# Performance work log

Hardware: AMD Instinct MI355X
Metric: run time of the kernel (lower is better)

The kernel has to match this reference:

```python
import jax, jax.numpy as jnp
import numpy as np
from jax import lax


def _lstm_layer(x, W_ih, W_hh, b_ih, b_hh):
    """Single LSTM layer, batch_first x: [B, T, in] -> (out [B,T,H], h_n [B,H], c_n [B,H]).
    PyTorch gate order: i, f, g, o."""
    B, T, _ = x.shape
    H = W_hh.shape[1]
    # Precompute input contributions for all timesteps (one big GEMM).
    xg = jnp.einsum('bti,gi->btg', x, W_ih) + b_ih + b_hh  # [B, T, 4H]
    h0 = jnp.zeros((B, H), dtype=x.dtype)
    c0 = jnp.zeros((B, H), dtype=x.dtype)

    def step(carry, g_t):
        h, c = carry
        gates = g_t + h @ W_hh.T  # [B, 4H]
        i, f, g, o = jnp.split(gates, 4, axis=-1)
        i = jax.nn.sigmoid(i)
        f = jax.nn.sigmoid(f)
        g = jnp.tanh(g)
        o = jax.nn.sigmoid(o)
        c = f * c + i * g
        h = o * jnp.tanh(c)
        return (h, c), h

    (h_n, c_n), hs = lax.scan(step, (h0, c0), jnp.swapaxes(xg, 0, 1))  # hs: [T, B, H]
    return jnp.swapaxes(hs, 0, 1), h_n, c_n


def setup_inputs() -> dict:
    key = jax.random.key(0)
    ks = jax.random.split(key, 12)
    H = 128
    IN = 1
    B, T = 256, 2048
    s = 1.0 / np.sqrt(H)  # PyTorch default init scale

    def u(k, shape):
        return jax.random.uniform(k, shape, jnp.float32, -s, s)

    return {
        'x': jax.random.normal(ks[0], (B, T, IN), jnp.float32),
        'W_ih_l0': u(ks[1], (4 * H, IN)),
        'W_hh_l0': u(ks[2], (4 * H, H)),
        'b_ih_l0': u(ks[3], (4 * H,)),
        'b_hh_l0': u(ks[4], (4 * H,)),
        'W_ih_l1': u(ks[5], (4 * H, H)),
        'W_hh_l1': u(ks[6], (4 * H, H)),
        'b_ih_l1': u(ks[7], (4 * H,)),
        'b_hh_l1': u(ks[8], (4 * H,)),
        'W_fc': u(ks[9], (1, H)),
        'b_fc': u(ks[10], (1,)),
    }


def reference(x, W_ih_l0, W_hh_l0, b_ih_l0, b_hh_l0,
              W_ih_l1, W_hh_l1, b_ih_l1, b_hh_l1, W_fc, b_fc):
    out0, h0, c0 = _lstm_layer(x, W_ih_l0, W_hh_l0, b_ih_l0, b_hh_l0)
    out1, h1, c1 = _lstm_layer(out0, W_ih_l1, W_hh_l1, b_ih_l1, b_hh_l1)
    last = out1[:, -1, :]                 # [B, H]
    y = last @ W_fc.T + b_fc              # [B, 1]
    h_n = jnp.stack([h0, h1], axis=0)     # [num_layers, B, H]
    c_n = jnp.stack([c0, c1], axis=0)
    return (y, h_n, c_n)
```

## Files before the change

### kernel.cpp

```cpp
#include <hip/hip_runtime.h>

#define T_SEQ 2048
#define HDIM  128
#define GDIM  512
#define BATCH 256

typedef _Float16 f16;
typedef _Float16 f16x2 __attribute__((ext_vector_type(2)));
typedef _Float16 f16x8 __attribute__((ext_vector_type(8)));

#if __has_builtin(__builtin_amdgcn_fdot2)
__device__ __forceinline__ float dot2(f16x2 a, f16x2 b, float c) {
    return __builtin_amdgcn_fdot2(a, b, c, false);
}
#else
__device__ __forceinline__ float dot2(f16x2 a, f16x2 b, float c) {
    return c + (float)a[0] * (float)b[0] + (float)a[1] * (float)b[1];
}
#endif

__device__ __forceinline__ f16x2 mk2(float a, float b) {
    f16x2 r; r[0] = (f16)a; r[1] = (f16)b; return r;
}
__device__ __forceinline__ f16x2 pr(f16x8 v, int m) {
    f16x2 r; r[0] = v[2 * m]; r[1] = v[2 * m + 1]; return r;
}

__device__ __forceinline__ float sigm(float x) {
    return __builtin_amdgcn_rcpf(1.0f + __expf(-x));
}
__device__ __forceinline__ float tanh_fast(float x) {
    float e = __expf(2.0f * x);
    return 1.0f - 2.0f * __builtin_amdgcn_rcpf(e + 1.0f);
}

__global__ __launch_bounds__(1024)
void lstm_fused(const float* __restrict__ x,
                const float* __restrict__ Wih0,
                const float* __restrict__ Whh0,
                const float* __restrict__ bih0,
                const float* __restrict__ bhh0,
                const float* __restrict__ Wih1,
                const float* __restrict__ Whh1,
                const float* __restrict__ bih1,
                const float* __restrict__ bhh1,
                const float* __restrict__ Wfc,
                const float* __restrict__ bfc,
                float* __restrict__ out)
{
    __shared__ __align__(16) float xs[T_SEQ];
    __shared__ __align__(16) f16   h0h[HDIM];
    __shared__ __align__(16) f16   h1h[HDIM];
    __shared__ float h0f[HDIM], h1f[HDIM];
    __shared__ float g0[GDIM];
    __shared__ float g1a[GDIM], g1b[GDIM];

    const int t  = threadIdx.x;
    const int b  = blockIdx.x;
    const bool gA = (t < 512);
    const int r  = t & 511;

    if (gA)
        ((float4*)xs)[t] = ((const float4*)(x + (size_t)b * T_SEQ))[t];

    f16x2 wa[64];
    f16x2 wb[32];
    {
        const float4* pa = (const float4*)((gA ? Whh0 : Wih1) + r * HDIM);
        const float4* pb = (const float4*)(Whh1 + r * HDIM + (gA ? 0 : 64));
#pragma unroll
        for (int c = 0; c < 32; ++c) {
            float4 v = pa[c];
            wa[2 * c]     = mk2(v.x, v.y);
            wa[2 * c + 1] = mk2(v.z, v.w);
        }
#pragma unroll
        for (int c = 0; c < 16; ++c) {
            float4 v = pb[c];
            wb[2 * c]     = mk2(v.x, v.y);
            wb[2 * c + 1] = mk2(v.z, v.w);
        }
    }
    const float xw   = gA ? Wih0[r] : 0.f;
    const float bias = gA ? (bih0[r] + bhh0[r]) : (bih1[r] + bhh1[r]);

    if (t < HDIM) {
        h0h[t] = (f16)0.f; h1h[t] = (f16)0.f;
        h0f[t] = 0.f;      h1f[t] = 0.f;
    }
    float c0r = 0.f, c1r = 0.f;
    __syncthreads();

    const f16x8* h0p  = (const f16x8*)h0h;
    const f16x8* hsel = ((const f16x8*)h1h) + (gA ? 0 : 8);

    for (int i = 0; i <= T_SEQ; ++i) {
        float sa = (i < T_SEQ ? xs[i] : 0.f) * xw + bias;
        float sb = 0.f, sc = 0.f, sd = 0.f;
#pragma unroll
        for (int c = 0; c < 16; ++c) {
            f16x8 h = h0p[c];
            sa = dot2(wa[4 * c + 0], pr(h, 0), sa);
            sb = dot2(wa[4 * c + 1], pr(h, 1), sb);
            sa = dot2(wa[4 * c + 2], pr(h, 2), sa);
            sb = dot2(wa[4 * c + 3], pr(h, 3), sb);
        }
#pragma unroll
        for (int c = 0; c < 8; ++c) {
            f16x8 h = hsel[c];
            sc = dot2(wb[4 * c + 0], pr(h, 0), sc);
            sd = dot2(wb[4 * c + 1], pr(h, 1), sd);
            sc = dot2(wb[4 * c + 2], pr(h, 2), sc);
            sd = dot2(wb[4 * c + 3], pr(h, 3), sd);
        }
        if (gA) {
            g0[r]  = sa + sb;
            g1a[r] = sc + sd;
        } else {
            g1b[r] = (sa + sb) + (sc + sd);
        }
        __syncthreads();

        if (t < 128) {
            if (i < T_SEQ) {
                float gi = sigm(g0[t]);
                float gf = sigm(g0[t + 128]);
                float gg = tanh_fast(g0[t + 256]);
                float go = sigm(g0[t + 384]);
                c0r = gf * c0r + gi * gg;
                float h = go * tanh_fast(c0r);
                h0h[t] = (f16)h;
                h0f[t] = h;
            }
        } else if (t >= 512 && t < 640) {
            if (i >= 1) {
                int j = t - 512;
                float gi = sigm(g1a[j]       + g1b[j]);
                float gf = sigm(g1a[j + 128] + g1b[j + 128]);
                float gg = tanh_fast(g1a[j + 256] + g1b[j + 256]);
                float go = sigm(g1a[j + 384] + g1b[j + 384]);
                c1r = gf * c1r + gi * gg;
                float h = go * tanh_fast(c1r);
                h1h[j] = (f16)h;
                h1f[j] = h;
            }
        }
        __syncthreads();
    }

    float* hn = out + BATCH;
    float* cn = out + BATCH + 2 * BATCH * HDIM;
    if (t < 128) {
        hn[(size_t)b * HDIM + t] = h0f[t];
        cn[(size_t)b * HDIM + t] = c0r;
    } else if (t >= 512 && t < 640) {
        int j = t - 512;
        hn[BATCH * HDIM + (size_t)b * HDIM + j] = h1f[j];
        cn[BATCH * HDIM + (size_t)b * HDIM + j] = c1r;
    }
    if (t < 64) {
        float p = h1f[t] * Wfc[t] + h1f[t + 64] * Wfc[t + 64];
#pragma unroll
        for (int o = 32; o >= 1; o >>= 1) p += __shfl_down(p, o);
        if (t == 0) out[b] = p + bfc[0];
    }
}

extern "C" void kernel_launch(void* const* d_in, const int* in_sizes, int n_in,
                              void* d_out, int out_size, void* d_ws, size_t ws_size,
                              hipStream_t stream) {
    const float* x    = (const float*)d_in[0];
    const float* Wih0 = (const float*)d_in[1];
    const float* Whh0 = (const float*)d_in[2];
    const float* bih0 = (const float*)d_in[3];
    const float* bhh0 = (const float*)d_in[4];
    const float* Wih1 = (const float*)d_in[5];
    const float* Whh1 = (const float*)d_in[6];
    const float* bih1 = (const float*)d_in[7];
    const float* bhh1 = (const float*)d_in[8];
    const float* Wfc  = (const float*)d_in[9];
    const float* bfc  = (const float*)d_in[10];
    lstm_fused<<<BATCH, 1024, 0, stream>>>(x, Wih0, Whh0, bih0, bhh0,
                                           Wih1, Whh1, bih1, bhh1,
                                           Wfc, bfc, (float*)d_out);
}
```

Baseline: 3.079 ms.

## Split fused two-layer LSTM into chunked per-layer kernels via workspace

Replaces the single 1024-thread fused kernel with two 512-thread kernels run per time chunk. Layer 0 also computes half of layer 1's input projection and stores it along with the other half of h0 in workspace. Layer 1 then consumes these with a one-step prefetch. Each kernel's recurrence now has a shorter per-step critical path on a smaller block with lower register pressure, so two blocks can share a CU. In exchange, the intermediates make a global-memory round trip and the layers no longer overlap within a block. The fused kernel remains as a fallback when the workspace is too small.

```diff
diff --git a/kernel.cpp b/kernel.cpp
--- a/kernel.cpp
+++ b/kernel.cpp
@@ -25,13 +25,235 @@
 __device__ __forceinline__ f16x2 pr(f16x8 v, int m) {
     f16x2 r; r[0] = v[2 * m]; r[1] = v[2 * m + 1]; return r;
 }
-
 __device__ __forceinline__ float sigm(float x) {
     return __builtin_amdgcn_rcpf(1.0f + __expf(-x));
 }
 __device__ __forceinline__ float tanh_fast(float x) {
     float e = __expf(2.0f * x);
     return 1.0f - 2.0f * __builtin_amdgcn_rcpf(e + 1.0f);
+}
+
+
+__global__ __launch_bounds__(512, 2)
+void lstm_l0(const float* __restrict__ x,
+             const float* __restrict__ Wih0,
+             const float* __restrict__ Whh0,
+             const float* __restrict__ bih0,
+             const float* __restrict__ bhh0,
+             const float* __restrict__ Wih1,
+             const float* __restrict__ bih1,
+             const float* __restrict__ bhh1,
+             float* __restrict__ h0s,  float* __restrict__ c0s,
+             float* __restrict__ xg1p, f16* __restrict__ h0hi,
+             int t0, int len, int first, int last,
+             float* __restrict__ out)
+{
+    __shared__ __align__(16) float xsc[T_SEQ];
+    __shared__ __align__(16) f16   h0h[HDIM];
+    __shared__ float h0f[HDIM];
+    __shared__ float g0[GDIM];
+
+    const int t = threadIdx.x;
+    const int b = blockIdx.x;
+
+    for (int idx = t; idx < len; idx += 512)
+        xsc[idx] = x[(size_t)b * T_SEQ + t0 + idx];
+
+    f16x2 wa[64];
+    f16x2 wb[32];
+    {
+        const float4* pa = (const float4*)(Whh0 + t * HDIM);
+        const float4* pb = (const float4*)(Wih1 + t * HDIM);
+#pragma unroll
+        for (int c = 0; c < 32; ++c) {
+            float4 v = pa[c];
+            wa[2 * c]     = mk2(v.x, v.y);
+            wa[2 * c + 1] = mk2(v.z, v.w);
+        }
+#pragma unroll
+        for (int c = 0; c < 16; ++c) {
+            float4 v = pb[c];
+            wb[2 * c]     = mk2(v.x, v.y);
+            wb[2 * c + 1] = mk2(v.z, v.w);
+        }
+    }
+    const float wx0   = Wih0[t];
+    const float bias0 = bih0[t] + bhh0[t];
+    const float b1    = bih1[t] + bhh1[t];
+
+    float c0r = 0.f;
+    if (t < HDIM) {
+        float h = first ? 0.f : h0s[b * HDIM + t];
+        if (!first) c0r = c0s[b * HDIM + t];
+        h0f[t] = h;
+        h0h[t] = (f16)h;
+    }
+    __syncthreads();
+
+    const f16x8* h0p = (const f16x8*)h0h;
+    float* xgB = xg1p + (size_t)b * len * 512;
+    f16*   hhB = h0hi + (size_t)b * len * 64;
+
+    for (int i = 0; i <= len; ++i) {
+        float s0a = (i < len ? xsc[i] : 0.f) * wx0 + bias0;
+        float s0b = 0.f, s0c = 0.f, s0d = 0.f;
+        float s1a = b1, s1b = 0.f;
+#pragma unroll
+        for (int c = 0; c < 16; ++c) {
+            f16x8 h = h0p[c];
+            s0a = dot2(wa[4 * c + 0], pr(h, 0), s0a);
+            s0b = dot2(wa[4 * c + 1], pr(h, 1), s0b);
+            s0c = dot2(wa[4 * c + 2], pr(h, 2), s0c);
+            s0d = dot2(wa[4 * c + 3], pr(h, 3), s0d);
+            if (c < 8) {
+                s1a = dot2(wb[4 * c + 0], pr(h, 0), s1a);
+                s1b = dot2(wb[4 * c + 1], pr(h, 1), s1b);
+                s1a = dot2(wb[4 * c + 2], pr(h, 2), s1a);
+                s1b = dot2(wb[4 * c + 3], pr(h, 3), s1b);
+            }
+        }
+        if (i < len) g0[t] = (s0a + s0b) + (s0c + s0d);
+        if (i >= 1)  xgB[(size_t)(i - 1) * 512 + t] = s1a + s1b;
+        __syncthreads();
+
+        if (t < 128 && i < len) {
+            float gi = sigm(g0[t]);
+            float gf = sigm(g0[t + 128]);
+            float gg = tanh_fast(g0[t + 256]);
+            float go = sigm(g0[t + 384]);
+            c0r = gf * c0r + gi * gg;
+            float h = go * tanh_fast(c0r);
+            h0h[t] = (f16)h;
+            h0f[t] = h;
+            if (t >= 64) hhB[(size_t)i * 64 + (t - 64)] = (f16)h;
+        }
+        __syncthreads();
+    }
+
+    if (t < 128) {
+        h0s[b * HDIM + t] = h0f[t];
+        c0s[b * HDIM + t] = c0r;
+        if (last) {
+            float* hn = out + BATCH;
+            float* cn = out + BATCH + 2 * BATCH * HDIM;
+            hn[(size_t)b * HDIM + t] = h0f[t];
+            cn[(size_t)b * HDIM + t] = c0r;
+        }
+    }
+}
+
+__global__ __launch_bounds__(512, 2)
+void lstm_l1(const float* __restrict__ Whh1,
+             const float* __restrict__ Wih1,
+             const float* __restrict__ Wfc,
+             const float* __restrict__ bfc,
+             float* __restrict__ h1s, float* __restrict__ c1s,
+             const float* __restrict__ xg1p, const f16* __restrict__ h0hi,
+             int len, int first, int last,
+             float* __restrict__ out)
+{
+    __shared__ __align__(16) f16   h1h[HDIM];
+    __shared__ float h1f[HDIM];
+    __shared__ float g1[GDIM];
+    __shared__ __align__(16) f16   hh[2][64];
+
+    const int t = threadIdx.x;
+    const int b = blockIdx.x;
+
+    f16x2 wa[64];
+    f16x2 wb[32];
+    {
+        const float4* pa = (const float4*)(Whh1 + t * HDIM);
+        const float4* pb = (const float4*)(Wih1 + t * HDIM + 64);
+#pragma unroll
+        for (int c = 0; c < 32; ++c) {
+            float4 v = pa[c];
+            wa[2 * c]     = mk2(v.x, v.y);
+            wa[2 * c + 1] = mk2(v.z, v.w);
+        }
+#pragma unroll
+        for (int c = 0; c < 16; ++c) {
+            float4 v = pb[c];
+            wb[2 * c]     = mk2(v.x, v.y);
+            wb[2 * c + 1] = mk2(v.z, v.w);
+        }
+    }
+
+    float c1r = 0.f;
+    if (t < HDIM) {
+        float h = first ? 0.f : h1s[b * HDIM + t];
+        if (!first) c1r = c1s[b * HDIM + t];
+        h1f[t] = h;
+        h1h[t] = (f16)h;
+    }
+
+    const float* xgB = xg1p + (size_t)b * len * 512;
+    const f16*   hB  = h0hi + (size_t)b * len * 64;
+    if (t < 8) ((f16x8*)hh[0])[t] = ((const f16x8*)hB)[t];
+    float xgv = xgB[t];
+    __syncthreads();
+
+    const f16x8* h1p = (const f16x8*)h1h;
+
+    for (int i = 0; i < len; ++i) {
+        float xgn = 0.f;
+        if (i + 1 < len) {
+            xgn = xgB[(size_t)(i + 1) * 512 + t];
+            if (t < 8)
+                ((f16x8*)hh[(i + 1) & 1])[t] =
+                    ((const f16x8*)(hB + (size_t)(i + 1) * 64))[t];
+        }
+        const f16x8* hhp = (const f16x8*)hh[i & 1];
+
+        float s1a = xgv, s1b = 0.f, s1c = 0.f, s1d = 0.f;
+#pragma unroll
+        for (int c = 0; c < 16; ++c) {
+            f16x8 h = h1p[c];
+            s1a = dot2(wa[4 * c + 0], pr(h, 0), s1a);
+            s1b = dot2(wa[4 * c + 1], pr(h, 1), s1b);
+            s1c = dot2(wa[4 * c + 2], pr(h, 2), s1c);
+            s1d = dot2(wa[4 * c + 3], pr(h, 3), s1d);
+            if (c < 8) {
+                f16x8 hx = hhp[c];
+                s1c = dot2(wb[4 * c + 0], pr(hx, 0), s1c);
+                s1d = dot2(wb[4 * c + 1], pr(hx, 1), s1d);
+                s1c = dot2(wb[4 * c + 2], pr(hx, 2), s1c);
+                s1d = dot2(wb[4 * c + 3], pr(hx, 3), s1d);
+            }
+        }
+        g1[t] = (s1a + s1b) + (s1c + s1d);
+        __syncthreads();
+
+        if (t < 128) {
+            float gi = sigm(g1[t]);
+            float gf = sigm(g1[t + 128]);
+            float gg = tanh_fast(g1[t + 256]);
+            float go = sigm(g1[t + 384]);
+            c1r = gf * c1r + gi * gg;
+            float h = go * tanh_fast(c1r);
+            h1h[t] = (f16)h;
+            h1f[t] = h;
+        }
+        __syncthreads();
+        xgv = xgn;
+    }
+
+    if (t < 128) {
+        h1s[b * HDIM + t] = h1f[t];
+        c1s[b * HDIM + t] = c1r;
+        if (last) {
+            float* hn = out + BATCH;
+            float* cn = out + BATCH + 2 * BATCH * HDIM;
+            hn[BATCH * HDIM + (size_t)b * HDIM + t] = h1f[t];
+            cn[BATCH * HDIM + (size_t)b * HDIM + t] = c1r;
+        }
+    }
+    if (last && t < 64) {
+        float p = h1f[t] * Wfc[t] + h1f[t + 64] * Wfc[t + 64];
+#pragma unroll
+        for (int o = 32; o >= 1; o >>= 1) p += __shfl_down(p, o);
+        if (t == 0) out[b] = p + bfc[0];
+    }
 }
 
 __global__ __launch_bounds__(1024)
@@ -113,12 +335,8 @@
             sc = dot2(wb[4 * c + 2], pr(h, 2), sc);
             sd = dot2(wb[4 * c + 3], pr(h, 3), sd);
         }
-        if (gA) {
-            g0[r]  = sa + sb;
-            g1a[r] = sc + sd;
-        } else {
-            g1b[r] = (sa + sb) + (sc + sd);
-        }
+        if (gA) { g0[r] = sa + sb; g1a[r] = sc + sd; }
+        else    { g1b[r] = (sa + sb) + (sc + sd); }
         __syncthreads();
 
         if (t < 128) {
@@ -180,7 +398,37 @@
     const float* bhh1 = (const float*)d_in[8];
     const float* Wfc  = (const float*)d_in[9];
     const float* bfc  = (const float*)d_in[10];
-    lstm_fused<<<BATCH, 1024, 0, stream>>>(x, Wih0, Whh0, bih0, bhh0,
-                                           Wih1, Whh1, bih1, bhh1,
-                                           Wfc, bfc, (float*)d_out);
-}
+    float* out = (float*)d_out;
+
+    const size_t stateB  = (size_t)4 * BATCH * HDIM * sizeof(float);
+    const size_t perStep = (size_t)BATCH * 512 * 4 + (size_t)BATCH * 64 * 2;
+    long long ch = 0;
+    if (d_ws && ws_size > stateB) ch = (long long)((ws_size - stateB) / perStep);
+    if (ch > T_SEQ) ch = T_SEQ;
+
+    if (ch >= 64) {
+        const int CH = (int)ch;
+        float* h0s  = (float*)d_ws;
+        float* c0s  = h0s + BATCH * HDIM;
+        float* h1s  = c0s + BATCH * HDIM;
+        float* c1s  = h1s + BATCH * HDIM;
+        float* xg1p = c1s + BATCH * HDIM;
+        f16*   h0hi = (f16*)(xg1p + (size_t)BATCH * CH * 512);
+        for (int t0 = 0; t0 < T_SEQ; t0 += CH) {
+            const int len   = (T_SEQ - t0 < CH) ? (T_SEQ - t0) : CH;
+            const int first = (t0 == 0);
+            const int last  = (t0 + len == T_SEQ);
+            lstm_l0<<<BATCH, 512, 0, stream>>>(x, Wih0, Whh0, bih0, bhh0,
+                                               Wih1, bih1, bhh1,
+                                               h0s, c0s, xg1p, h0hi,
+                                               t0, len, first, last, out);
+            lstm_l1<<<BATCH, 512, 0, stream>>>(Whh1, Wih1, Wfc, bfc,
+                                               h1s, c1s, xg1p, h0hi,
+                                               len, first, last, out);
+        }
+    } else {
+        lstm_fused<<<BATCH, 1024, 0, stream>>>(x, Wih0, Whh0, bih0, bhh0,
+                                               Wih1, Whh1, bih1, bhh1,
+                                               Wfc, bfc, out);
+    }
+}
```

After: 3.464 ms. 12.5% more time.

## Use 512-thread blocks with weights split across registers, LDS and global

Applied to the files above, without the earlier changes.

Each block now runs with 512 threads instead of 1024. Every thread computes one gate row for both layers, so a single sum per layer replaces the cross-half partial-sum exchange. The layer-1 weights are spread across three places: registers, a padded LDS tile, and a pre-packed fp16 global buffer built by a small prep kernel and streamed from L2 with software prefetch. The goal is more work per thread and fewer threads per barrier. The cost is higher register pressure, about 140KB of LDS per block, and extra global loads inside the serial time loop.

```diff
diff --git a/kernel.cpp b/kernel.cpp
--- a/kernel.cpp
+++ b/kernel.cpp
@@ -4,6 +4,8 @@
 #define HDIM  128
 #define GDIM  512
 #define BATCH 256
+#define GW_PLANES 8
+#define WS_NEED (GW_PLANES * GDIM * 16)
 
 typedef _Float16 f16;
 typedef _Float16 f16x2 __attribute__((ext_vector_type(2)));
@@ -25,7 +27,12 @@
 __device__ __forceinline__ f16x2 pr(f16x8 v, int m) {
     f16x2 r; r[0] = v[2 * m]; r[1] = v[2 * m + 1]; return r;
 }
-
+__device__ __forceinline__ f16x8 pk8(float4 u, float4 v) {
+    f16x8 w;
+    w[0] = (f16)u.x; w[1] = (f16)u.y; w[2] = (f16)u.z; w[3] = (f16)u.w;
+    w[4] = (f16)v.x; w[5] = (f16)v.y; w[6] = (f16)v.z; w[7] = (f16)v.w;
+    return w;
+}
 __device__ __forceinline__ float sigm(float x) {
     return __builtin_amdgcn_rcpf(1.0f + __expf(-x));
 }
@@ -34,19 +41,210 @@
     return 1.0f - 2.0f * __builtin_amdgcn_rcpf(e + 1.0f);
 }
 
+__global__ void prep_pack(const float* __restrict__ Whh1, f16x8* __restrict__ wg)
+{
+    const int c = blockIdx.x;
+    const int t = threadIdx.x;
+    const float4* s = (const float4*)(Whh1 + t * HDIM + 64 + 8 * c);
+    wg[c * GDIM + t] = pk8(s[0], s[1]);
+}
+
+__global__ __launch_bounds__(512, 2)
+void lstm_fused_v6(const float* __restrict__ x,
+                   const float* __restrict__ Wih0,
+                   const float* __restrict__ Whh0,
+                   const float* __restrict__ bih0,
+                   const float* __restrict__ bhh0,
+                   const float* __restrict__ Wih1,
+                   const float* __restrict__ Whh1,
+                   const float* __restrict__ bih1,
+                   const float* __restrict__ bhh1,
+                   const float* __restrict__ Wfc,
+                   const float* __restrict__ bfc,
+                   const f16x8* __restrict__ wg,
+                   float* __restrict__ out)
+{
+    __shared__ __align__(16) f16x8 wlds[GDIM * 17];
+    __shared__ __align__(16) float xs[T_SEQ];
+    __shared__ __align__(16) f16   h0h[HDIM];
+    __shared__ __align__(16) f16   h1h[HDIM];
+    __shared__ float h0f[HDIM], h1f[HDIM];
+    __shared__ float g0[GDIM], g1[GDIM];
+
+    const int t = threadIdx.x;
+    const int b = blockIdx.x;
+
+    ((float4*)xs)[t] = ((const float4*)(x + (size_t)b * T_SEQ))[t];
+
+    f16x2 w0[64];
+    f16x2 wi[32];
+    {
+        const float4* p0 = (const float4*)(Whh0 + t * HDIM);
+        const float4* p1 = (const float4*)(Wih1 + t * HDIM);
+#pragma unroll
+        for (int c = 0; c < 32; ++c) {
+            float4 v = p0[c];
+            w0[2 * c]     = mk2(v.x, v.y);
+            w0[2 * c + 1] = mk2(v.z, v.w);
+        }
+#pragma unroll
+        for (int c = 0; c < 16; ++c) {
+            float4 v = p1[c];
+            wi[2 * c]     = mk2(v.x, v.y);
+            wi[2 * c + 1] = mk2(v.z, v.w);
+        }
+    }
+    f16x8* wrow = wlds + t * 17;
+    {
+        const float4* p = (const float4*)(Wih1 + t * HDIM + 64);
+#pragma unroll
+        for (int c = 0; c < 8; ++c) wrow[c] = pk8(p[2 * c], p[2 * c + 1]);
+        p = (const float4*)(Whh1 + t * HDIM);
+#pragma unroll
+        for (int c = 0; c < 8; ++c) wrow[8 + c] = pk8(p[2 * c], p[2 * c + 1]);
+    }
+    const float wx0   = Wih0[t];
+    const float bias0 = bih0[t] + bhh0[t];
+    const float bias1 = bih1[t] + bhh1[t];
+
+    if (t < HDIM) {
+        h0h[t] = (f16)0.f; h1h[t] = (f16)0.f;
+        h0f[t] = 0.f;      h1f[t] = 0.f;
+    }
+    float c0r = 0.f, c1r = 0.f;
+    __syncthreads();
+
+    const f16x8* h0p = (const f16x8*)h0h;
+    const f16x8* h1p = (const f16x8*)h1h;
+
+    for (int i = 0; i <= T_SEQ; ++i) {
+        int z = 0;
+        asm volatile("" : "+v"(z));
+        const f16x8* wr  = wrow + z;
+        const f16x8* wg2 = wg + z;
+
+        f16x8 ga = wg2[0 * GDIM + t];
+        f16x8 gb = wg2[1 * GDIM + t];
+
+        float s0a = (i < T_SEQ ? xs[i] : 0.f) * wx0 + bias0;
+        float s0b = 0.f, s0c = 0.f, s0d = 0.f;
+        float s1a = bias1, s1b = 0.f;
+
+#pragma unroll
+        for (int c = 0; c < 8; ++c) {
+            f16x8 h = h0p[c];
+            s0a = dot2(w0[4 * c + 0], pr(h, 0), s0a);
+            s0b = dot2(w0[4 * c + 1], pr(h, 1), s0b);
+            s0c = dot2(w0[4 * c + 2], pr(h, 2), s0c);
+            s0d = dot2(w0[4 * c + 3], pr(h, 3), s0d);
+            s1a = dot2(wi[4 * c + 0], pr(h, 0), s1a);
+            s1b = dot2(wi[4 * c + 1], pr(h, 1), s1b);
+            s1a = dot2(wi[4 * c + 2], pr(h, 2), s1a);
+            s1b = dot2(wi[4 * c + 3], pr(h, 3), s1b);
+        }
+#pragma unroll
+        for (int c = 0; c < 8; ++c) {
+            f16x8 h  = h0p[8 + c];
+            f16x8 lw = wr[c];
+            s0a = dot2(w0[32 + 4 * c + 0], pr(h, 0), s0a);
+            s0b = dot2(w0[32 + 4 * c + 1], pr(h, 1), s0b);
+            s0c = dot2(w0[32 + 4 * c + 2], pr(h, 2), s0c);
+            s0d = dot2(w0[32 + 4 * c + 3], pr(h, 3), s0d);
+            s1a = dot2(pr(lw, 0), pr(h, 0), s1a);
+            s1b = dot2(pr(lw, 1), pr(h, 1), s1b);
+            s1a = dot2(pr(lw, 2), pr(h, 2), s1a);
+            s1b = dot2(pr(lw, 3), pr(h, 3), s1b);
+        }
+#pragma unroll
+        for (int c = 0; c < 8; ++c) {
+            f16x8 h  = h1p[c];
+            f16x8 lw = wr[8 + c];
+            s1a = dot2(pr(lw, 0), pr(h, 0), s1a);
+            s1b = dot2(pr(lw, 1), pr(h, 1), s1b);
+            s1a = dot2(pr(lw, 2), pr(h, 2), s1a);
+            s1b = dot2(pr(lw, 3), pr(h, 3), s1b);
+        }
+#pragma unroll
+        for (int bb = 0; bb < 4; ++bb) {
+            f16x8 na = ga, nb = gb;
+            if (bb < 3) {
+                na = wg2[(2 * bb + 2) * GDIM + t];
+                nb = wg2[(2 * bb + 3) * GDIM + t];
+            }
+            f16x8 h = h1p[8 + 2 * bb];
+            s1a = dot2(pr(ga, 0), pr(h, 0), s1a);
+            s1b = dot2(pr(ga, 1), pr(h, 1), s1b);
+            s1a = dot2(pr(ga, 2), pr(h, 2), s1a);
+            s1b = dot2(pr(ga, 3), pr(h, 3), s1b);
+            h = h1p[9 + 2 * bb];
+            s1a = dot2(pr(gb, 0), pr(h, 0), s1a);
+            s1b = dot2(pr(gb, 1), pr(h, 1), s1b);
+            s1a = dot2(pr(gb, 2), pr(h, 2), s1a);
+            s1b = dot2(pr(gb, 3), pr(h, 3), s1b);
+            ga = na; gb = nb;
+        }
+        g0[t] = (s0a + s0b) + (s0c + s0d);
+        g1[t] = s1a + s1b;
+        __syncthreads();
+
+        if (t < 128) {
+            if (i < T_SEQ) {
+                float gi = sigm(g0[t]);
+                float gf = sigm(g0[t + 128]);
+                float gg = tanh_fast(g0[t + 256]);
+                float go = sigm(g0[t + 384]);
+                c0r = gf * c0r + gi * gg;
+                float h = go * tanh_fast(c0r);
+                h0h[t] = (f16)h;
+                h0f[t] = h;
+            }
+        } else if (t < 256) {
+            if (i >= 1) {
+                int j = t - 128;
+                float gi = sigm(g1[j]);
+                float gf = sigm(g1[j + 128]);
+                float gg = tanh_fast(g1[j + 256]);
+                float go = sigm(g1[j + 384]);
+                c1r = gf * c1r + gi * gg;
+                float h = go * tanh_fast(c1r);
+                h1h[j] = (f16)h;
+                h1f[j] = h;
+            }
+        }
+        __syncthreads();
+    }
+
+    float* hn = out + BATCH;
+    float* cn = out + BATCH + 2 * BATCH * HDIM;
+    if (t < 128) {
+        hn[(size_t)b * HDIM + t] = h0f[t];
+        cn[(size_t)b * HDIM + t] = c0r;
+    } else if (t < 256) {
+        int j = t - 128;
+        hn[BATCH * HDIM + (size_t)b * HDIM + j] = h1f[j];
+        cn[BATCH * HDIM + (size_t)b * HDIM + j] = c1r;
+    }
+    if (t < 64) {
+        float p = h1f[t] * Wfc[t] + h1f[t + 64] * Wfc[t + 64];
+#pragma unroll
+        for (int o = 32; o >= 1; o >>= 1) p += __shfl_down(p, o);
+        if (t == 0) out[b] = p + bfc[0];
+    }
+}
+
 __global__ __launch_bounds__(1024)
-void lstm_fused(const float* __restrict__ x,
-                const float* __restrict__ Wih0,
-                const float* __restrict__ Whh0,
-                const float* __restrict__ bih0,
-                const float* __restrict__ bhh0,
-                const float* __restrict__ Wih1,
-                const float* __restrict__ Whh1,
-                const float* __restrict__ bih1,
-                const float* __restrict__ bhh1,
-                const float* __restrict__ Wfc,
-                const float* __restrict__ bfc,
-                float* __restrict__ out)
+void lstm_fused_fb(const float* __restrict__ x,
+                   const float* __restrict__ Wih0,
+                   const float* __restrict__ Whh0,
+                   const float* __restrict__ bih0,
+                   const float* __restrict__ bhh0,
+                   const float* __restrict__ Wih1,
+                   const float* __restrict__ Whh1,
+                   const float* __restrict__ bih1,
+                   const float* __restrict__ bhh1,
+                   const float* __restrict__ Wfc,
+                   const float* __restrict__ bfc,
+                   float* __restrict__ out)
 {
     __shared__ __align__(16) float xs[T_SEQ];
     __shared__ __align__(16) f16   h0h[HDIM];
@@ -113,12 +311,8 @@
             sc = dot2(wb[4 * c + 2], pr(h, 2), sc);
             sd = dot2(wb[4 * c + 3], pr(h, 3), sd);
         }
-        if (gA) {
-            g0[r]  = sa + sb;
-            g1a[r] = sc + sd;
-        } else {
-            g1b[r] = (sa + sb) + (sc + sd);
-        }
+        if (gA) { g0[r] = sa + sb; g1a[r] = sc + sd; }
+        else    { g1b[r] = (sa + sb) + (sc + sd); }
         __syncthreads();
 
         if (t < 128) {
@@ -180,7 +374,17 @@
     const float* bhh1 = (const float*)d_in[8];
     const float* Wfc  = (const float*)d_in[9];
     const float* bfc  = (const float*)d_in[10];
-    lstm_fused<<<BATCH, 1024, 0, stream>>>(x, Wih0, Whh0, bih0, bhh0,
-                                           Wih1, Whh1, bih1, bhh1,
-                                           Wfc, bfc, (float*)d_out);
-}
+    float* out = (float*)d_out;
+
+    if (d_ws && ws_size >= (size_t)WS_NEED) {
+        f16x8* wg = (f16x8*)d_ws;
+        prep_pack<<<GW_PLANES, GDIM, 0, stream>>>(Whh1, wg);
+        lstm_fused_v6<<<BATCH, GDIM, 0, stream>>>(x, Wih0, Whh0, bih0, bhh0,
+                                                  Wih1, Whh1, bih1, bhh1,
+                                                  Wfc, bfc, wg, out);
+    } else {
+        lstm_fused_fb<<<BATCH, 1024, 0, stream>>>(x, Wih0, Whh0, bih0, bhh0,
+                                                  Wih1, Whh1, bih1, bhh1,
+                                                  Wfc, bfc, out);
+    }
+}
```

Result: faster. 2.964 ms (-3.7%).

## Split LSTM layers into producer/consumer blocks linked by a global-memory FIFO

Applied to the files above, without the earlier changes.

Replaces the single 1024-thread block per batch row with two 512-thread blocks per row: one runs layer 0 and also computes the first half of layer 1's input projection, and the other runs layer 1's recurrence. The two communicate through a 32-deep ring buffer in workspace memory with atomic producer/consumer counters. The aim is to take layer 1 off layer 0's critical path, shorten each block's per-step barrier chain, and run two blocks per CU. The cost is global-memory traffic, spin-waiting, and reliance on both blocks of a pair being co-resident, or the spin-waits deadlock. If the workspace is too small, the old kernel runs as a fallback.

```diff
diff --git a/kernel.cpp b/kernel.cpp
--- a/kernel.cpp
+++ b/kernel.cpp
@@ -5,6 +5,11 @@
 #define GDIM  512
 #define BATCH 256
 
+#define DEPTH    32
+#define SLOT_DW  576
+#define FLAGS_DW 8192
+#define WS_NEED  ((size_t)(FLAGS_DW + (size_t)BATCH * DEPTH * SLOT_DW) * 4)
+
 typedef _Float16 f16;
 typedef _Float16 f16x2 __attribute__((ext_vector_type(2)));
 typedef _Float16 f16x8 __attribute__((ext_vector_type(8)));
@@ -25,7 +30,6 @@
 __device__ __forceinline__ f16x2 pr(f16x8 v, int m) {
     f16x2 r; r[0] = v[2 * m]; r[1] = v[2 * m + 1]; return r;
 }
-
 __device__ __forceinline__ float sigm(float x) {
     return __builtin_amdgcn_rcpf(1.0f + __expf(-x));
 }
@@ -34,19 +38,235 @@
     return 1.0f - 2.0f * __builtin_amdgcn_rcpf(e + 1.0f);
 }
 
+__device__ __forceinline__ uint ldv(const uint* p) {
+    return __hip_atomic_load(p, __ATOMIC_RELAXED, __HIP_MEMORY_SCOPE_AGENT);
+}
+__device__ __forceinline__ void stv(uint* p, uint v) {
+    __hip_atomic_store(p, v, __ATOMIC_RELAXED, __HIP_MEMORY_SCOPE_AGENT);
+}
+
+__global__ __launch_bounds__(512, 2)
+void lstm_pc(const float* __restrict__ x,
+             const float* __restrict__ Wih0,
+             const float* __restrict__ Whh0,
+             const float* __restrict__ bih0,
+             const float* __restrict__ bhh0,
+             const float* __restrict__ Wih1,
+             const float* __restrict__ Whh1,
+             const float* __restrict__ bih1,
+             const float* __restrict__ bhh1,
+             const float* __restrict__ Wfc,
+             const float* __restrict__ bfc,
+             uint* __restrict__ ws,
+             float* __restrict__ out)
+{
+    __shared__ __align__(16) float xs[T_SEQ];
+    __shared__ __align__(16) f16   hsh[HDIM];
+    __shared__ float hsf[HDIM];
+    __shared__ float g[GDIM];
+    __shared__ __align__(16) f16   hh[2][64];
+
+    const int t    = threadIdx.x;
+    const int b    = blockIdx.x >> 1;
+    const int role = blockIdx.x & 1;
+    uint* prod = ws + b * 16;
+    uint* cons = ws + 4096 + b * 16;
+    uint* fif  = ws + FLAGS_DW + (size_t)b * (DEPTH * SLOT_DW);
+
+    float cr = 0.f;
+    if (t < HDIM) { hsh[t] = (f16)0.f; hsf[t] = 0.f; }
+
+    if (role == 0) {
+        ((float4*)xs)[t] = ((const float4*)(x + (size_t)b * T_SEQ))[t];
+        f16x2 wa[64];
+        f16x2 wb[32];
+        {
+            const float4* pa = (const float4*)(Whh0 + t * HDIM);
+            const float4* pb = (const float4*)(Wih1 + t * HDIM);
+#pragma unroll
+            for (int c = 0; c < 32; ++c) {
+                float4 v = pa[c];
+                wa[2*c]   = mk2(v.x, v.y);
+                wa[2*c+1] = mk2(v.z, v.w);
+            }
+#pragma unroll
+            for (int c = 0; c < 16; ++c) {
+                float4 v = pb[c];
+                wb[2*c]   = mk2(v.x, v.y);
+                wb[2*c+1] = mk2(v.z, v.w);
+            }
+        }
+        const float wx0   = Wih0[t];
+        const float bias0 = bih0[t] + bhh0[t];
+        const float b1    = bih1[t] + bhh1[t];
+        const f16x8* hp = (const f16x8*)hsh;
+        int consv = 0;
+
+        for (int i = 0; i <= T_SEQ; ++i) {
+            asm volatile("s_waitcnt vmcnt(0)" ::: "memory");
+            __syncthreads();
+            if (t == 0) {
+                if (i >= 2)
+                    __hip_atomic_store(prod, (uint)(i - 1), __ATOMIC_RELEASE,
+                                       __HIP_MEMORY_SCOPE_AGENT);
+                if (consv < i - 30)
+                    do { consv = (int)ldv(cons); } while (consv < i - 30);
+            }
+            float s0a = (i < T_SEQ ? xs[i] : 0.f) * wx0 + bias0;
+            float s0b = 0.f, s0c = 0.f, s0d = 0.f;
+            float s1a = b1, s1b = 0.f;
+#pragma unroll
+            for (int c = 0; c < 16; ++c) {
+                f16x8 h = hp[c];
+                s0a = dot2(wa[4*c+0], pr(h,0), s0a);
+                s0b = dot2(wa[4*c+1], pr(h,1), s0b);
+                s0c = dot2(wa[4*c+2], pr(h,2), s0c);
+                s0d = dot2(wa[4*c+3], pr(h,3), s0d);
+                if (c < 8) {
+                    s1a = dot2(wb[4*c+0], pr(h,0), s1a);
+                    s1b = dot2(wb[4*c+1], pr(h,1), s1b);
+                    s1a = dot2(wb[4*c+2], pr(h,2), s1a);
+                    s1b = dot2(wb[4*c+3], pr(h,3), s1b);
+                }
+            }
+            if (i >= 1)
+                stv(&fif[((i-1) & (DEPTH-1)) * SLOT_DW + t],
+                    __float_as_uint(s1a + s1b));
+            if (i < T_SEQ) g[t] = (s0a + s0b) + (s0c + s0d);
+            __syncthreads();
+            if (t < 128 && i < T_SEQ) {
+                float gi = sigm(g[t]);
+                float gf = sigm(g[t + 128]);
+                float gg = tanh_fast(g[t + 256]);
+                float go = sigm(g[t + 384]);
+                cr = gf * cr + gi * gg;
+                float h = go * tanh_fast(cr);
+                hsh[t] = (f16)h; hsf[t] = h;
+                if (t >= 64)
+                    stv(&fif[(i & (DEPTH-1)) * SLOT_DW + 512 + (t - 64)],
+                        __float_as_uint(h));
+            }
+            __syncthreads();
+        }
+        asm volatile("s_waitcnt vmcnt(0)" ::: "memory");
+        __syncthreads();
+        if (t == 0)
+            __hip_atomic_store(prod, (uint)T_SEQ, __ATOMIC_RELEASE,
+                               __HIP_MEMORY_SCOPE_AGENT);
+        if (t < 128) {
+            out[BATCH + (size_t)b * HDIM + t] = hsf[t];
+            out[BATCH + 2 * BATCH * HDIM + (size_t)b * HDIM + t] = cr;
+        }
+    } else {
+        f16x2 wa[64];
+        f16x2 wb[32];
+        {
+            const float4* pa = (const float4*)(Whh1 + t * HDIM);
+            const float4* pb = (const float4*)(Wih1 + t * HDIM + 64);
+#pragma unroll
+            for (int c = 0; c < 32; ++c) {
+                float4 v = pa[c];
+                wa[2*c]   = mk2(v.x, v.y);
+                wa[2*c+1] = mk2(v.z, v.w);
+            }
+#pragma unroll
+            for (int c = 0; c < 16; ++c) {
+                float4 v = pb[c];
+                wb[2*c]   = mk2(v.x, v.y);
+                wb[2*c+1] = mk2(v.z, v.w);
+            }
+        }
+        int pc = 0;
+        if (t == 501) {
+            do {
+                pc = (int)__hip_atomic_load(prod, __ATOMIC_ACQUIRE,
+                                            __HIP_MEMORY_SCOPE_AGENT);
+            } while (pc < 2);
+        }
+        __syncthreads();
+        uint xgc = ldv(&fif[t]);
+        if (t >= 448)
+            hh[0][t - 448] = (f16)__uint_as_float(ldv(&fif[512 + (t - 448)]));
+        __syncthreads();
+        const f16x8* hp = (const f16x8*)hsh;
+
+        for (int j = 0; j < T_SEQ; ++j) {
+            uint xgn = 0u; float hnv = 0.f;
+            if (j + 1 < T_SEQ) {
+                const int s = ((j + 1) & (DEPTH - 1)) * SLOT_DW;
+                xgn = ldv(&fif[s + t]);
+                if (t >= 448)
+                    hnv = __uint_as_float(ldv(&fif[s + 512 + (t - 448)]));
+            }
+            const f16x8* hx = (const f16x8*)hh[j & 1];
+            float s1a = __uint_as_float(xgc), s1b = 0.f, s1c = 0.f, s1d = 0.f;
+#pragma unroll
+            for (int c = 0; c < 16; ++c) {
+                f16x8 h = hp[c];
+                s1a = dot2(wa[4*c+0], pr(h,0), s1a);
+                s1b = dot2(wa[4*c+1], pr(h,1), s1b);
+                s1c = dot2(wa[4*c+2], pr(h,2), s1c);
+                s1d = dot2(wa[4*c+3], pr(h,3), s1d);
+                if (c < 8) {
+                    f16x8 hq = hx[c];
+                    s1c = dot2(wb[4*c+0], pr(hq,0), s1c);
+                    s1d = dot2(wb[4*c+1], pr(hq,1), s1d);
+                    s1c = dot2(wb[4*c+2], pr(hq,2), s1c);
+                    s1d = dot2(wb[4*c+3], pr(hq,3), s1d);
+                }
+            }
+            g[t] = (s1a + s1b) + (s1c + s1d);
+            __syncthreads();
+            if (t < 128) {
+                float gi = sigm(g[t]);
+                float gf = sigm(g[t + 128]);
+                float gg = tanh_fast(g[t + 256]);
+                float go = sigm(g[t + 384]);
+                cr = gf * cr + gi * gg;
+                float h = go * tanh_fast(cr);
+                hsh[t] = (f16)h; hsf[t] = h;
+            } else if (t >= 448) {
+                hh[(j + 1) & 1][t - 448] = (f16)hnv;
+            }
+            if (t == 500) stv(cons, (uint)(j + 1));
+            if (t == 501) {
+                int need = j + 3; if (need > T_SEQ) need = T_SEQ;
+                if (pc < need) {
+                    do {
+                        pc = (int)__hip_atomic_load(prod, __ATOMIC_ACQUIRE,
+                                                    __HIP_MEMORY_SCOPE_AGENT);
+                    } while (pc < need);
+                }
+            }
+            __syncthreads();
+            xgc = xgn;
+        }
+        if (t < 128) {
+            out[BATCH + BATCH * HDIM + (size_t)b * HDIM + t] = hsf[t];
+            out[BATCH + 2 * BATCH * HDIM + BATCH * HDIM + (size_t)b * HDIM + t] = cr;
+        }
+        if (t < 64) {
+            float p = hsf[t] * Wfc[t] + hsf[t + 64] * Wfc[t + 64];
+#pragma unroll
+            for (int o = 32; o >= 1; o >>= 1) p += __shfl_down(p, o);
+            if (t == 0) out[b] = p + bfc[0];
+        }
+    }
+}
+
 __global__ __launch_bounds__(1024)
-void lstm_fused(const float* __restrict__ x,
-                const float* __restrict__ Wih0,
-                const float* __restrict__ Whh0,
-                const float* __restrict__ bih0,
-                const float* __restrict__ bhh0,
-                const float* __restrict__ Wih1,
-                const float* __restrict__ Whh1,
-                const float* __restrict__ bih1,
-                const float* __restrict__ bhh1,
-                const float* __restrict__ Wfc,
-                const float* __restrict__ bfc,
-                float* __restrict__ out)
+void lstm_fused_fb(const float* __restrict__ x,
+                   const float* __restrict__ Wih0,
+                   const float* __restrict__ Whh0,
+                   const float* __restrict__ bih0,
+                   const float* __restrict__ bhh0,
+                   const float* __restrict__ Wih1,
+                   const float* __restrict__ Whh1,
+                   const float* __restrict__ bih1,
+                   const float* __restrict__ bhh1,
+                   const float* __restrict__ Wfc,
+                   const float* __restrict__ bfc,
+                   float* __restrict__ out)
 {
     __shared__ __align__(16) float xs[T_SEQ];
     __shared__ __align__(16) f16   h0h[HDIM];
@@ -71,14 +291,14 @@
 #pragma unroll
         for (int c = 0; c < 32; ++c) {
             float4 v = pa[c];
-            wa[2 * c]     = mk2(v.x, v.y);
-            wa[2 * c + 1] = mk2(v.z, v.w);
+            wa[2*c]   = mk2(v.x, v.y);
+            wa[2*c+1] = mk2(v.z, v.w);
         }
 #pragma unroll
         for (int c = 0; c < 16; ++c) {
             float4 v = pb[c];
-            wb[2 * c]     = mk2(v.x, v.y);
-            wb[2 * c + 1] = mk2(v.z, v.w);
+            wb[2*c]   = mk2(v.x, v.y);
+            wb[2*c+1] = mk2(v.z, v.w);
         }
     }
     const float xw   = gA ? Wih0[r] : 0.f;
@@ -100,25 +320,21 @@
 #pragma unroll
         for (int c = 0; c < 16; ++c) {
             f16x8 h = h0p[c];
-            sa = dot2(wa[4 * c + 0], pr(h, 0), sa);
-            sb = dot2(wa[4 * c + 1], pr(h, 1), sb);
-            sa = dot2(wa[4 * c + 2], pr(h, 2), sa);
-            sb = dot2(wa[4 * c + 3], pr(h, 3), sb);
+            sa = dot2(wa[4*c+0], pr(h,0), sa);
+            sb = dot2(wa[4*c+1], pr(h,1), sb);
+            sa = dot2(wa[4*c+2], pr(h,2), sa);
+            sb = dot2(wa[4*c+3], pr(h,3), sb);
         }
 #pragma unroll
         for (int c = 0; c < 8; ++c) {
             f16x8 h = hsel[c];
-            sc = dot2(wb[4 * c + 0], pr(h, 0), sc);
-            sd = dot2(wb[4 * c + 1], pr(h, 1), sd);
-            sc = dot2(wb[4 * c + 2], pr(h, 2), sc);
-            sd = dot2(wb[4 * c + 3], pr(h, 3), sd);
-        }
-        if (gA) {
-            g0[r]  = sa + sb;
-            g1a[r] = sc + sd;
-        } else {
-            g1b[r] = (sa + sb) + (sc + sd);
-        }
+            sc = dot2(wb[4*c+0], pr(h,0), sc);
+            sd = dot2(wb[4*c+1], pr(h,1), sd);
+            sc = dot2(wb[4*c+2], pr(h,2), sc);
+            sd = dot2(wb[4*c+3], pr(h,3), sd);
+        }
+        if (gA) { g0[r] = sa + sb; g1a[r] = sc + sd; }
+        else    { g1b[r] = (sa + sb) + (sc + sd); }
         __syncthreads();
 
         if (t < 128) {
@@ -180,7 +396,16 @@
     const float* bhh1 = (const float*)d_in[8];
     const float* Wfc  = (const float*)d_in[9];
     const float* bfc  = (const float*)d_in[10];
-    lstm_fused<<<BATCH, 1024, 0, stream>>>(x, Wih0, Whh0, bih0, bhh0,
-                                           Wih1, Whh1, bih1, bhh1,
-                                           Wfc, bfc, (float*)d_out);
-}
+    float* out = (float*)d_out;
+
+    if (d_ws && ws_size >= WS_NEED) {
+        hipMemsetAsync(d_ws, 0, FLAGS_DW * 4, stream);
+        lstm_pc<<<2 * BATCH, GDIM, 0, stream>>>(x, Wih0, Whh0, bih0, bhh0,
+                                                Wih1, Whh1, bih1, bhh1,
+                                                Wfc, bfc, (uint*)d_ws, out);
+    } else {
+        lstm_fused_fb<<<BATCH, 1024, 0, stream>>>(x, Wih0, Whh0, bih0, bhh0,
+                                                  Wih1, Whh1, bih1, bhh1,
+                                                  Wfc, bfc, out);
+    }
+}
```

Measured after the change: 8.728 ms. 183% more time.
